# Kernel optimization log

Hardware: AMD Instinct MI355X
Metric: run time of the kernel (lower is better)

The kernel has to match this reference:

```python
import jax, jax.numpy as jnp
import numpy as np

HID = 768          # args.hidden_size
LSTM2 = 768        # args.lstm_dim * 2
SCALE = HID ** -0.5


def _cross_attn(q_in, kv_in, Wq, bq, Wk, bk, Wv, bv):
    # Linear projections (weights stored as [in, out])
    Q = q_in @ Wq + bq            # [B, Sq, H]
    K = kv_in @ Wk + bk           # [B, Sk, H]
    V = kv_in @ Wv + bv           # [B, Sk, H]
    attn = jnp.einsum('bqh,bkh->bqk', Q, K) * SCALE
    attn = jax.nn.softmax(attn, axis=-1)
    return jnp.einsum('bqk,bkh->bqh', attn, V)


def setup_inputs() -> dict:
    key = jax.random.key(0)
    ks = jax.random.split(key, 14)
    B, Ssyn, Ssem = 4, 4096, 2048
    syntactic_feat = jax.random.normal(ks[0], (B, Ssyn, LSTM2), jnp.float32)
    semantic_feat = jax.random.normal(ks[1], (B, Ssem, HID), jnp.float32)

    def lin(k, fan_in, fan_out):
        kw, kb = jax.random.split(k)
        bound = 1.0 / np.sqrt(fan_in)
        W = jax.random.uniform(kw, (fan_in, fan_out), jnp.float32, -bound, bound)
        b = jax.random.uniform(kb, (fan_out,), jnp.float32, -bound, bound)
        return W, b

    # syntax_to_semantic: query_dim=HID, key_dim=LSTM2
    Wq1, bq1 = lin(ks[2], HID, HID)
    Wk1, bk1 = lin(ks[3], LSTM2, HID)
    Wv1, bv1 = lin(ks[4], LSTM2, HID)
    # semantic_to_syntax: query_dim=LSTM2, key_dim=HID
    Wq2, bq2 = lin(ks[5], LSTM2, HID)
    Wk2, bk2 = lin(ks[6], HID, HID)
    Wv2, bv2 = lin(ks[7], HID, HID)
    return dict(syntactic_feat=syntactic_feat, semantic_feat=semantic_feat,
                Wq1=Wq1, bq1=bq1, Wk1=Wk1, bk1=bk1, Wv1=Wv1, bv1=bv1,
                Wq2=Wq2, bq2=bq2, Wk2=Wk2, bk2=bk2, Wv2=Wv2, bv2=bv2)


def reference(syntactic_feat, semantic_feat,
              Wq1, bq1, Wk1, bk1, Wv1, bv1,
              Wq2, bq2, Wk2, bk2, Wv2, bv2):
    # enhanced_semantic: queries from semantic, keys/values from syntactic
    enhanced_semantic = _cross_attn(semantic_feat, syntactic_feat,
                                    Wq1, bq1, Wk1, bk1, Wv1, bv1)
    # enhanced_syntax: queries from syntactic, keys/values from semantic
    enhanced_syntax = _cross_attn(syntactic_feat, semantic_feat,
                                  Wq2, bq2, Wk2, bk2, Wv2, bv2)
    return enhanced_semantic, enhanced_syntax
```

## Files before the change

kernel.cpp:

```cpp
#include <hip/hip_runtime.h>
#include <stdint.h>


typedef unsigned short u16;
typedef __attribute__((ext_vector_type(8))) __bf16 bf16x8;
typedef __attribute__((ext_vector_type(4))) float f32x4;

__device__ __forceinline__ float bf2f(u16 u) {
  union { unsigned int i; float f; } x; x.i = ((unsigned int)u) << 16; return x.f;
}
__device__ __forceinline__ u16 f2bf(float f) {
  union { float f; unsigned int i; } x; x.f = f;
  unsigned int i = x.i;
  i += 0x7fffu + ((i >> 16) & 1u);
  return (u16)(i >> 16);
}

__device__ __forceinline__ void cp16(void* lds, const void* g) {
  __builtin_amdgcn_global_load_lds((__attribute__((address_space(1))) void*)g,
                                   (__attribute__((address_space(3))) void*)lds,
                                   16, 0, 0);
}

struct GemmDesc {
  const u16* A; const u16* Bt; const float* bias; void* C;
  long sA, sB, sC;
  int K, lda, ldb, ldc;
  int gx, gy;
  int start;
  int mode, outf;
  float scale;
};
struct GemmPack { GemmDesc d[6]; int nd; };

#define PHASE(MH, NH, PAR, STAGE, WAITC)                                      \
  {                                                                           \
    const bf16x8* As8 =                                                       \
        (const bf16x8*)((const char*)L + (PAR) * 32768 + (MH) * 16384);       \
    const bf16x8* Bs8 =                                                       \
        (const bf16x8*)((const char*)L + 65536 + (PAR) * 32768 + (NH) * 16384);\
    bf16x8 a0[2][4], b0[2][2];                                                \
    _Pragma("unroll")                                                         \
    for (int s = 0; s < 2; ++s) {                                             \
      _Pragma("unroll")                                                       \
      for (int i = 0; i < 4; ++i) a0[s][i] = As8[iaq[s][i]];                  \
      _Pragma("unroll")                                                       \
      for (int j = 0; j < 2; ++j) b0[s][j] = Bs8[ibq[s][j]];                  \
    }                                                                         \
    STAGE;                                                                    \
    __builtin_amdgcn_s_barrier();                                             \
    asm volatile("s_waitcnt lgkmcnt(0)" ::: "memory");                        \
    __builtin_amdgcn_s_setprio(1);                                            \
    _Pragma("unroll")                                                         \
    for (int s = 0; s < 2; ++s)                                               \
      _Pragma("unroll")                                                       \
      for (int i = 0; i < 4; ++i)                                             \
        _Pragma("unroll")                                                     \
        for (int j = 0; j < 2; ++j)                                           \
          acc[MH][NH][i][j] = __builtin_amdgcn_mfma_f32_16x16x32_bf16(        \
              b0[s][j], a0[s][i], acc[MH][NH][i][j], 0, 0, 0);                \
    __builtin_amdgcn_s_setprio(0);                                            \
    WAITC;                                                                    \
    __builtin_amdgcn_s_barrier();                                             \
  }

__global__ __launch_bounds__(512, 2)
void gemm256_kernel(GemmPack p)
{
  __shared__ __align__(16) u16 L[65536];

  int seg = 0;
#pragma unroll
  for (int t = 1; t < 6; ++t)
    if (t < p.nd && (int)blockIdx.x >= p.d[t].start) seg = t;
  const GemmDesc& g = p.d[seg];
  const int local = (int)blockIdx.x - g.start;
  const int pxy = g.gx * g.gy;
  const int bz = local / pxy;
  const int rem = local - bz * pxy;
  const int by = rem / g.gx;
  const int bx = rem - by * g.gx;

  const int tid  = threadIdx.x;
  const int lane = tid & 63;
  const int wave = tid >> 6;
  const int l15  = lane & 15;
  const int quad = lane >> 4;
  const int wm   = wave >> 2;
  const int wn   = wave & 3;

  const char* Ab = (const char*)(g.A + (long)bz * g.sA + (long)bx * 256 * g.lda);
  const char* Bb = (const char*)(g.Bt + (long)bz * g.sB + (long)by * 256 * g.ldb);
  const long ldaB = (long)g.lda * 2;
  const long ldbB = (long)g.ldb * 2;

  const int gchk = (lane & 7) ^ (lane >> 3);
  const char* pa0 = Ab + (long)(wave * 8 + (lane >> 3)) * ldaB + (gchk << 4);
  const char* pb0 = Bb + (long)(wave * 8 + (lane >> 3)) * ldbB + (gchk << 4);
  char* lA = (char*)L + wave * 1024;
  char* lB = (char*)L + 65536 + wave * 1024;

  auto stageA = [&](int par, int h, int kt) {
    char* d = lA + par * 32768 + h * 16384;
    const char* s = pa0 + (long)h * 128 * ldaB + ((long)kt << 7);
    cp16(d, s);
    cp16(d + 8192, s + 64 * ldaB);
  };
  auto stageB = [&](int par, int h, int kt) {
    char* d = lB + par * 32768 + h * 16384;
    const char* s = pb0 + (long)h * 128 * ldbB + ((long)kt << 7);
    cp16(d, s);
    cp16(d + 8192, s + 64 * ldbB);
  };

  int iaq[2][4], ibq[2][2];
#pragma unroll
  for (int s = 0; s < 2; ++s) {
#pragma unroll
    for (int i = 0; i < 4; ++i)
      iaq[s][i] = (wm * 64 + i * 16 + l15) * 8 + ((s * 4 + quad) ^ (l15 & 7));
#pragma unroll
    for (int j = 0; j < 2; ++j)
      ibq[s][j] = (wn * 32 + j * 16 + l15) * 8 + ((s * 4 + quad) ^ (l15 & 7));
  }

  f32x4 acc[2][2][4][2];
  {
    f32x4 zz = {0.f, 0.f, 0.f, 0.f};
#pragma unroll
    for (int mh = 0; mh < 2; ++mh)
#pragma unroll
      for (int nh = 0; nh < 2; ++nh)
#pragma unroll
        for (int i = 0; i < 4; ++i)
#pragma unroll
          for (int j = 0; j < 2; ++j) acc[mh][nh][i][j] = zz;
  }

  stageA(0, 0, 0); stageB(0, 0, 0);
  stageA(0, 1, 0); stageB(0, 1, 0);
  stageA(1, 0, 1); stageB(1, 0, 1);
  asm volatile("s_waitcnt vmcnt(4)" ::: "memory");
  __builtin_amdgcn_s_barrier();

  const int NI = g.K >> 7;
  for (int it = 0; it < NI; ++it) {
    const int t = it * 2;
    const bool more = (it + 1) < NI;
    PHASE(0, 0, 0, stageA(1, 1, t + 1), )
    PHASE(0, 1, 0, stageB(1, 1, t + 1), )
    PHASE(1, 0, 0, if (more) stageA(0, 0, t + 2), )
    PHASE(1, 1, 0, if (more) stageB(0, 0, t + 2),
          if (more) { asm volatile("s_waitcnt vmcnt(4)" ::: "memory"); }
          else      { asm volatile("s_waitcnt vmcnt(0)" ::: "memory"); })
    PHASE(0, 0, 1, if (more) stageA(0, 1, t + 2), )
    PHASE(0, 1, 1, if (more) stageB(0, 1, t + 2), )
    PHASE(1, 0, 1, if (more) stageA(1, 0, t + 3), )
    PHASE(1, 1, 1, if (more) stageB(1, 0, t + 3),
          if (more) { asm volatile("s_waitcnt vmcnt(4)" ::: "memory"); })
  }

  const long cbase = (long)bz * g.sC;
#pragma unroll
  for (int mh = 0; mh < 2; ++mh) {
#pragma unroll
    for (int i = 0; i < 4; ++i) {
      const int row = bx * 256 + mh * 128 + wm * 64 + i * 16 + l15;
      const float rbias = (g.mode == 2) ? g.bias[row] : 0.f;
#pragma unroll
      for (int nh = 0; nh < 2; ++nh) {
#pragma unroll
        for (int j = 0; j < 2; ++j) {
          const int colbase = by * 256 + nh * 128 + wn * 32 + j * 16 + quad * 4;
          float v[4];
#pragma unroll
          for (int r = 0; r < 4; ++r) v[r] = acc[mh][nh][i][j][r] * g.scale;
          if (g.mode == 1) {
            const float4 cb = *(const float4*)(g.bias + colbase);
            v[0] += cb.x; v[1] += cb.y; v[2] += cb.z; v[3] += cb.w;
          } else if (g.mode == 2) {
#pragma unroll
            for (int r = 0; r < 4; ++r) v[r] += rbias;
          }
          const long idx = cbase + (long)row * g.ldc + colbase;
          if (g.outf) {
            float4 st; st.x = v[0]; st.y = v[1]; st.z = v[2]; st.w = v[3];
            *(float4*)((float*)g.C + idx) = st;
          } else {
            uint2 st;
            st.x = (unsigned int)f2bf(v[0]) | ((unsigned int)f2bf(v[1]) << 16);
            st.y = (unsigned int)f2bf(v[2]) | ((unsigned int)f2bf(v[3]) << 16);
            *(uint2*)((u16*)g.C + idx) = st;
          }
        }
      }
    }
  }
}

__global__ __launch_bounds__(256)
void cvt2_bf16_kernel(const float* __restrict__ sa, u16* __restrict__ da, int n8a,
                      const float* __restrict__ sb, u16* __restrict__ db, int n8b)
{
  int idx = blockIdx.x * 256 + threadIdx.x;
  const float* src; u16* dst; int i;
  if (idx < n8a) { src = sa; dst = da; i = idx; }
  else           { src = sb; dst = db; i = idx - n8a; if (i >= n8b) return; }
  const float4* s4 = (const float4*)src;
  float4 a = s4[i * 2], b = s4[i * 2 + 1];
  uint4 o;
  o.x = (unsigned int)f2bf(a.x) | ((unsigned int)f2bf(a.y) << 16);
  o.y = (unsigned int)f2bf(a.z) | ((unsigned int)f2bf(a.w) << 16);
  o.z = (unsigned int)f2bf(b.x) | ((unsigned int)f2bf(b.y) << 16);
  o.w = (unsigned int)f2bf(b.z) | ((unsigned int)f2bf(b.w) << 16);
  ((uint4*)dst)[i] = o;
}

__global__ void transpose6_kernel(const float* s0, const float* s1, const float* s2,
                                  const float* s3, const float* s4, const float* s5,
                                  u16* d0, u16* d1, u16* d2,
                                  u16* d3, u16* d4, u16* d5)
{
  __shared__ float t[32][33];
  const float* src; u16* dst;
  switch (blockIdx.z) {
    case 0: src = s0; dst = d0; break;
    case 1: src = s1; dst = d1; break;
    case 2: src = s2; dst = d2; break;
    case 3: src = s3; dst = d3; break;
    case 4: src = s4; dst = d4; break;
    default: src = s5; dst = d5; break;
  }
  const int tx = threadIdx.x, ty = threadIdx.y;
  const int x = blockIdx.x * 32 + tx;
  const int y0 = blockIdx.y * 32;
#pragma unroll
  for (int j = 0; j < 32; j += 8) t[ty + j][tx] = src[(long)(y0 + ty + j) * 768 + x];
  __syncthreads();
  const int x2 = y0 + tx;
#pragma unroll
  for (int j = 0; j < 32; j += 8)
    dst[(long)(blockIdx.x * 32 + ty + j) * 768 + x2] = f2bf(t[tx][ty + j]);
}

template <int NV>
__device__ __forceinline__ void softmax_row(u16* row)
{
  __shared__ float red[8];
  const int tid  = threadIdx.x;
  const int lane = tid & 63;
  const int wave = tid >> 6;
  uint4* p4 = (uint4*)row;

  uint4 ld[NV / 8];
#pragma unroll
  for (int c = 0; c < NV / 8; ++c) ld[c] = p4[tid + c * 256];
  float v[NV];
#pragma unroll
  for (int c = 0; c < NV / 8; ++c) {
    unsigned int w[4] = {ld[c].x, ld[c].y, ld[c].z, ld[c].w};
#pragma unroll
    for (int q = 0; q < 4; ++q) {
      v[c * 8 + q * 2]     = bf2f((u16)(w[q] & 0xffffu));
      v[c * 8 + q * 2 + 1] = bf2f((u16)(w[q] >> 16));
    }
  }

  float m = -1e30f;
#pragma unroll
  for (int i = 0; i < NV; ++i) m = fmaxf(m, v[i]);
#pragma unroll
  for (int off = 32; off > 0; off >>= 1) m = fmaxf(m, __shfl_xor(m, off, 64));
  if (lane == 0) red[wave] = m;
  __syncthreads();
  m = fmaxf(fmaxf(red[0], red[1]), fmaxf(red[2], red[3]));

  float s = 0.f;
#pragma unroll
  for (int i = 0; i < NV; ++i) { v[i] = __expf(v[i] - m); s += v[i]; }
#pragma unroll
  for (int off = 32; off > 0; off >>= 1) s += __shfl_xor(s, off, 64);
  if (lane == 0) red[4 + wave] = s;
  __syncthreads();
  s = (red[4] + red[5]) + (red[6] + red[7]);
  const float inv = 1.0f / s;

#pragma unroll
  for (int c = 0; c < NV / 8; ++c) {
    unsigned int w[4];
#pragma unroll
    for (int q = 0; q < 4; ++q) {
      const u16 lo = f2bf(v[c * 8 + q * 2] * inv);
      const u16 hi = f2bf(v[c * 8 + q * 2 + 1] * inv);
      w[q] = (unsigned int)lo | ((unsigned int)hi << 16);
    }
    uint4 st; st.x = w[0]; st.y = w[1]; st.z = w[2]; st.w = w[3];
    p4[tid + c * 256] = st;
  }
}

__global__ __launch_bounds__(256)
void softmax_both_kernel(u16* S1, u16* S2, const u16* cpy_src, u16* cpy_dst)
{
  if (blockIdx.x < 8192) { softmax_row<16>(S1 + (long)blockIdx.x * 4096); return; }
  if (blockIdx.x < 24576) { softmax_row<8>(S2 + (long)(blockIdx.x - 8192) * 2048); return; }
  const long base = (long)(blockIdx.x - 24576) * 512 + threadIdx.x;
  const uint4* s = (const uint4*)cpy_src;
  uint4* d = (uint4*)cpy_dst;
  d[base] = s[base];
  d[base + 256] = s[base + 256];
}


static GemmDesc mkdesc(const void* A, const void* Bt, const float* bias, void* C,
                       long sA, long sB, long sC, int K, int lda, int ldb, int ldc,
                       int M, int N, int start, int mode, int outf, float scale)
{
  GemmDesc d;
  d.A = (const u16*)A; d.Bt = (const u16*)Bt; d.bias = bias; d.C = C;
  d.sA = sA; d.sB = sB; d.sC = sC;
  d.K = K; d.lda = lda; d.ldb = ldb; d.ldc = ldc;
  d.gx = M / 256; d.gy = N / 256; d.start = start;
  d.mode = mode; d.outf = outf; d.scale = scale;
  return d;
}

extern "C" void kernel_launch(void* const* d_in, const int* in_sizes, int n_in,
                              void* d_out, int out_size, void* d_ws, size_t ws_size,
                              hipStream_t stream)
{
  (void)in_sizes; (void)n_in; (void)out_size; (void)ws_size;
  const float* syn = (const float*)d_in[0];
  const float* sem = (const float*)d_in[1];
  const float* W[6]    = {(const float*)d_in[2], (const float*)d_in[4],  (const float*)d_in[6],
                          (const float*)d_in[8], (const float*)d_in[10], (const float*)d_in[12]};
  const float* bias[6] = {(const float*)d_in[3], (const float*)d_in[5],  (const float*)d_in[7],
                          (const float*)d_in[9], (const float*)d_in[11], (const float*)d_in[13]};
  float* out = (float*)d_out;

  u16* ws   = (u16*)d_ws;
  u16* S1   = ws;
  u16* synb = ws;
  u16* semb = ws + 12582912;
  u16* WT   = ws + 18874368;
  u16* S2   = ws + 33554432;
  u16* V1T  = ws + 67108864;
  u16* Q1   = ws + 79691776;
  u16* V2Tc = ws + 79691776;
  u16* K1  = (u16*)out;
  u16* o1  = (u16*)(out + 6291456);
  u16* Q2  = o1;
  u16* K2  = o1 + 12582912;
  u16* V2T = o1 + 18874368;

  const float SC = 0.036084391824351615f;

  cvt2_bf16_kernel<<<dim3(9216), dim3(256), 0, stream>>>(
      syn, synb, 1572864, sem, semb, 786432);

  transpose6_kernel<<<dim3(24, 24, 6), dim3(32, 8, 1), 0, stream>>>(
      W[0], W[1], W[2], W[3], W[4], W[5],
      WT + 0 * 589824, WT + 1 * 589824, WT + 2 * 589824,
      WT + 3 * 589824, WT + 4 * 589824, WT + 5 * 589824);

  {
    GemmPack p; p.nd = 6;
    p.d[0] = mkdesc(synb, WT + 1 * 589824, bias[1], K1, 0, 0, 0,
                    768, 768, 768, 768, 16384, 768, 0, 1, 0, 1.f);
    p.d[1] = mkdesc(synb, WT + 3 * 589824, bias[3], Q2, 0, 0, 0,
                    768, 768, 768, 768, 16384, 768, 192, 1, 0, 1.f);
    p.d[2] = mkdesc(WT + 2 * 589824, synb, bias[2], V1T, 0, 0, 0,
                    768, 768, 768, 16384, 768, 16384, 384, 2, 0, 1.f);
    p.d[3] = mkdesc(semb, WT + 0 * 589824, bias[0], Q1, 0, 0, 0,
                    768, 768, 768, 768, 8192, 768, 576, 1, 0, 1.f);
    p.d[4] = mkdesc(semb, WT + 4 * 589824, bias[4], K2, 0, 0, 0,
                    768, 768, 768, 768, 8192, 768, 672, 1, 0, 1.f);
    p.d[5] = mkdesc(WT + 5 * 589824, semb, bias[5], V2T, 0, 0, 0,
                    768, 768, 768, 8192, 768, 8192, 768, 2, 0, 1.f);
    gemm256_kernel<<<dim3(864), dim3(512), 0, stream>>>(p);
  }

  {
    GemmPack p; p.nd = 2;
    p.d[0] = mkdesc(Q1, K1, nullptr, S1,
                    1572864L, 3145728L, 8388608L,
                    768, 768, 768, 4096, 2048, 4096, 0, 0, 0, SC);
    p.d[1] = mkdesc(Q2, K2, nullptr, S2,
                    3145728L, 1572864L, 8388608L,
                    768, 768, 768, 2048, 4096, 2048, 512, 0, 0, SC);
    gemm256_kernel<<<dim3(1024), dim3(512), 0, stream>>>(p);
  }

  softmax_both_kernel<<<dim3(26112), dim3(256), 0, stream>>>(S1, S2, V2T, V2Tc);

  {
    GemmPack p; p.nd = 2;
    p.d[0] = mkdesc(S1, V1T, nullptr, out,
                    8388608L, 4096L, 1572864L,
                    4096, 4096, 16384, 768, 2048, 768, 0, 0, 1, 1.f);
    p.d[1] = mkdesc(S2, V2Tc, nullptr, out + 6291456,
                    8388608L, 2048L, 3145728L,
                    2048, 2048, 8192, 768, 4096, 768, 96, 0, 1, 1.f);
    gemm256_kernel<<<dim3(288), dim3(512), 0, stream>>>(p);
  }
}
```

Baseline: 600.9 us.

## Hold full B fragments in registers per tile and reorder GEMM staging schedule

The 256x256 GEMM main loop now loads both N-halves of the B operand from LDS into registers once per K tile and reuses them across four phases that each cover half of an M-half's rows. The aim is to cut redundant LDS reads of B. The global-to-LDS staging order is reshuffled so B tiles are issued ahead of A, with adjusted vmcnt waits. This raises register pressure from the persistent B fragments and changes how tightly load/compute overlap is timed.

Measured after the change: 566.3 us. 1.06x faster.

```diff
diff --git a/kernel.cpp b/kernel.cpp
--- a/kernel.cpp
+++ b/kernel.cpp
@@ -33,32 +33,45 @@
 };
 struct GemmPack { GemmDesc d[6]; int nd; };
 
-#define PHASE(MH, NH, PAR, STAGE, WAITC)                                      \
+#define PHASE(MH, I0, PAR, RDB, STAGE, WAITC)                                 \
   {                                                                           \
     const bf16x8* As8 =                                                       \
         (const bf16x8*)((const char*)L + (PAR) * 32768 + (MH) * 16384);       \
-    const bf16x8* Bs8 =                                                       \
-        (const bf16x8*)((const char*)L + 65536 + (PAR) * 32768 + (NH) * 16384);\
-    bf16x8 a0[2][4], b0[2][2];                                                \
+    bf16x8 a0[2][2];                                                          \
     _Pragma("unroll")                                                         \
-    for (int s = 0; s < 2; ++s) {                                             \
+    for (int s = 0; s < 2; ++s)                                               \
       _Pragma("unroll")                                                       \
-      for (int i = 0; i < 4; ++i) a0[s][i] = As8[iaq[s][i]];                  \
+      for (int i = 0; i < 2; ++i) a0[s][i] = As8[iaq[s][(I0) + i]];           \
+    if (RDB) {                                                                \
+      const bf16x8* Bl8 =                                                     \
+          (const bf16x8*)((const char*)L + 65536 + (PAR) * 32768);            \
+      const bf16x8* Bh8 =                                                     \
+          (const bf16x8*)((const char*)L + 65536 + (PAR) * 32768 + 16384);    \
       _Pragma("unroll")                                                       \
-      for (int j = 0; j < 2; ++j) b0[s][j] = Bs8[ibq[s][j]];                  \
+      for (int s = 0; s < 2; ++s)                                             \
+        _Pragma("unroll")                                                     \
+        for (int j = 0; j < 2; ++j) {                                         \
+          bfr[0][s][j] = Bl8[ibq[s][j]];                                      \
+          bfr[1][s][j] = Bh8[ibq[s][j]];                                      \
+        }                                                                     \
     }                                                                         \
     STAGE;                                                                    \
+    if (RDB) { asm volatile("s_waitcnt lgkmcnt(8)" ::: "memory"); }           \
     __builtin_amdgcn_s_barrier();                                             \
     asm volatile("s_waitcnt lgkmcnt(0)" ::: "memory");                        \
     __builtin_amdgcn_s_setprio(1);                                            \
     _Pragma("unroll")                                                         \
     for (int s = 0; s < 2; ++s)                                               \
       _Pragma("unroll")                                                       \
-      for (int i = 0; i < 4; ++i)                                             \
+      for (int i = 0; i < 2; ++i)                                             \
         _Pragma("unroll")                                                     \
-        for (int j = 0; j < 2; ++j)                                           \
-          acc[MH][NH][i][j] = __builtin_amdgcn_mfma_f32_16x16x32_bf16(        \
-              b0[s][j], a0[s][i], acc[MH][NH][i][j], 0, 0, 0);                \
+        for (int nh = 0; nh < 2; ++nh)                                        \
+          _Pragma("unroll")                                                   \
+          for (int j = 0; j < 2; ++j)                                         \
+            acc[MH][nh][(I0) + i][j] =                                        \
+                __builtin_amdgcn_mfma_f32_16x16x32_bf16(                      \
+                    bfr[nh][s][j], a0[s][i], acc[MH][nh][(I0) + i][j],        \
+                    0, 0, 0);                                                 \
     __builtin_amdgcn_s_setprio(0);                                            \
     WAITC;                                                                    \
     __builtin_amdgcn_s_barrier();                                             \
@@ -100,15 +113,15 @@
   char* lA = (char*)L + wave * 1024;
   char* lB = (char*)L + 65536 + wave * 1024;
 
-  auto stageA = [&](int par, int h, int kt) {
-    char* d = lA + par * 32768 + h * 16384;
-    const char* s = pa0 + (long)h * 128 * ldaB + ((long)kt << 7);
+  auto stA = [&](int tile, int h) {
+    char* d = lA + (tile & 1) * 32768 + h * 16384;
+    const char* s = pa0 + (long)h * 128 * ldaB + ((long)tile << 7);
     cp16(d, s);
     cp16(d + 8192, s + 64 * ldaB);
   };
-  auto stageB = [&](int par, int h, int kt) {
-    char* d = lB + par * 32768 + h * 16384;
-    const char* s = pb0 + (long)h * 128 * ldbB + ((long)kt << 7);
+  auto stB = [&](int tile, int h) {
+    char* d = lB + (tile & 1) * 32768 + h * 16384;
+    const char* s = pb0 + (long)h * 128 * ldbB + ((long)tile << 7);
     cp16(d, s);
     cp16(d + 8192, s + 64 * ldbB);
   };
@@ -136,28 +149,31 @@
 #pragma unroll
           for (int j = 0; j < 2; ++j) acc[mh][nh][i][j] = zz;
   }
-
-  stageA(0, 0, 0); stageB(0, 0, 0);
-  stageA(0, 1, 0); stageB(0, 1, 0);
-  stageA(1, 0, 1); stageB(1, 0, 1);
-  asm volatile("s_waitcnt vmcnt(4)" ::: "memory");
+  bf16x8 bfr[2][2][2];
+
+  stB(0, 0); stB(0, 1); stA(0, 0); stA(0, 1);
+  stB(1, 0); stB(1, 1); stA(1, 0);
+  asm volatile("s_waitcnt vmcnt(6)" ::: "memory");
   __builtin_amdgcn_s_barrier();
 
-  const int NI = g.K >> 7;
+  const int nt = g.K >> 6;
+  const int NI = nt >> 1;
   for (int it = 0; it < NI; ++it) {
     const int t = it * 2;
-    const bool more = (it + 1) < NI;
-    PHASE(0, 0, 0, stageA(1, 1, t + 1), )
-    PHASE(0, 1, 0, stageB(1, 1, t + 1), )
-    PHASE(1, 0, 0, if (more) stageA(0, 0, t + 2), )
-    PHASE(1, 1, 0, if (more) stageB(0, 0, t + 2),
-          if (more) { asm volatile("s_waitcnt vmcnt(4)" ::: "memory"); }
-          else      { asm volatile("s_waitcnt vmcnt(0)" ::: "memory"); })
-    PHASE(0, 0, 1, if (more) stageA(0, 1, t + 2), )
-    PHASE(0, 1, 1, if (more) stageB(0, 1, t + 2), )
-    PHASE(1, 0, 1, if (more) stageA(1, 0, t + 3), )
-    PHASE(1, 1, 1, if (more) stageB(1, 0, t + 3),
-          if (more) { asm volatile("s_waitcnt vmcnt(4)" ::: "memory"); })
+    const bool m2 = (t + 2) < nt;
+    const bool m3 = (t + 3) < nt;
+    PHASE(0, 0, 0, 1, stA(t + 1, 1), )
+    PHASE(0, 2, 0, 0, if (m2) stB(t + 2, 0), )
+    PHASE(1, 0, 0, 0, if (m2) stB(t + 2, 1), )
+    PHASE(1, 2, 0, 0, if (m2) stA(t + 2, 0),
+          if (m2) { asm volatile("s_waitcnt vmcnt(6)" ::: "memory"); }
+          else    { asm volatile("s_waitcnt vmcnt(0)" ::: "memory"); })
+    PHASE(0, 0, 1, 1, if (m2) stA(t + 2, 1), )
+    PHASE(0, 2, 1, 0, if (m3) stB(t + 3, 0), )
+    PHASE(1, 0, 1, 0, if (m3) stB(t + 3, 1), )
+    PHASE(1, 2, 1, 0, if (m3) stA(t + 3, 0),
+          if (m3)      { asm volatile("s_waitcnt vmcnt(6)" ::: "memory"); }
+          else if (m2) { asm volatile("s_waitcnt vmcnt(0)" ::: "memory"); })
   }
 
   const long cbase = (long)bz * g.sC;
```
